# Optimization experiments

Hardware: AMD Instinct MI355X
Metric: run time of the kernel (lower is better)

## Reference

```python
import jax, jax.numpy as jnp
import numpy as np

H = 32        # num query heads
KVH = 8       # num kv heads
D = 128       # head_dim
ROPE_BASE = 10000.0
NEG_INF = jnp.finfo(jnp.float32).min


def rope_interleaved(x):
    """Interleaved (GPT-NeoX-style pairs (x0,x1),(x2,x3),...) RoPE. x: [b,s,h,d]."""
    d = x.shape[-1]
    inv_freq = 1.0 / (ROPE_BASE ** (jnp.arange(0, d, 2, dtype=jnp.float32) / d))  # [d/2]
    pos = jnp.arange(x.shape[1], dtype=jnp.float32)
    ang = pos[:, None] * inv_freq[None, :]                    # [s, d/2]
    cos = jnp.cos(ang)[None, :, None, :]
    sin = jnp.sin(ang)[None, :, None, :]
    xp = x.reshape(*x.shape[:-1], d // 2, 2)
    x1, x2 = xp[..., 0], xp[..., 1]
    r1 = x1 * cos - x2 * sin
    r2 = x1 * sin + x2 * cos
    return jnp.stack([r1, r2], axis=-1).reshape(x.shape)


def setup_inputs() -> dict:
    key = jax.random.key(0)
    k1, k2, k3 = jax.random.split(key, 3)
    B, S, E = 2, 2048, 4096
    x = jax.random.normal(k1, (B, S, E), dtype=jnp.float32)
    wqkv = jax.random.normal(k2, (E + 2 * KVH * D, E), dtype=jnp.float32) * 0.02
    wo = jax.random.normal(k3, (E, E), dtype=jnp.float32) * 0.02
    return {"x": x, "wqkv": wqkv, "wo": wo}


def reference(x, wqkv, wo):
    b, s, e = x.shape
    q_per_kv = H // KVH
    # fused QKV projection (torch Linear layout: y = x @ W.T)
    qkv = jnp.einsum('bse,fe->bsf', x, wqkv)
    # rearrange 'b s (h gs d) -> b s h gs d', gs = q_per_kv + 2
    qkv = qkv.reshape(b, s, KVH, q_per_kv + 2, D)
    q = qkv[..., :q_per_kv, :].reshape(b, s, H, D)   # (h gs) -> H query heads
    k = qkv[..., -2, :]                              # [b,s,KVH,D]
    v = qkv[..., -1, :]
    # RoPE (rotary_emb_dim == head_dim, interleaved)
    q = rope_interleaved(q)
    k = rope_interleaved(k)
    # GQA: expand kv heads to match query heads
    k = jnp.repeat(k, q_per_kv, axis=2)              # [b,s,H,D]
    v = jnp.repeat(v, q_per_kv, axis=2)
    scale = D ** -0.5
    scores = jnp.einsum('bqhd,bkhd->bhqk', q, k) * scale
    causal = jnp.tril(jnp.ones((s, s), dtype=bool))
    scores = jnp.where(causal[None, None], scores, NEG_INF)
    attn = jax.nn.softmax(scores, axis=-1)
    ctx = jnp.einsum('bhqk,bkhd->bqhd', attn, v).reshape(b, s, H * D)
    return jnp.einsum('bsf,ef->bse', ctx, wo)
```

## Files before the change

### kernel.cpp

```cpp
#include <hip/hip_runtime.h>
#include <cstdint>

typedef __bf16 bf16;
typedef __bf16 bf16x8 __attribute__((ext_vector_type(8)));
typedef float  f32x4  __attribute__((ext_vector_type(4)));

#define AS1(p) ((__attribute__((address_space(1))) void*)(p))
#define AS3(p) ((__attribute__((address_space(3))) void*)(p))

__device__ __forceinline__ void gload16(const void* g, void* l) {
  __builtin_amdgcn_global_load_lds(AS1(g), AS3(l), 16, 0, 0);
}

constexpr int B_ = 2, S_ = 2048, E_ = 4096, H_ = 32, KVH_ = 8, D_ = 128;
constexpr int QPK_ = H_ / KVH_;
constexpr int F_ = E_ + 2 * KVH_ * D_;
constexpr int M_ = B_ * S_;

__global__ void f2bf_k(const float* __restrict__ in, bf16* __restrict__ out, int n8) {
  int i = blockIdx.x * 256 + threadIdx.x;
  if (i >= n8) return;
  const float4* p = (const float4*)(in + (size_t)i * 8);
  float4 a = p[0], b = p[1];
  bf16x8 o;
  o[0] = (bf16)a.x; o[1] = (bf16)a.y; o[2] = (bf16)a.z; o[3] = (bf16)a.w;
  o[4] = (bf16)b.x; o[5] = (bf16)b.y; o[6] = (bf16)b.z; o[7] = (bf16)b.w;
  *(bf16x8*)(out + (size_t)i * 8) = o;
}

__global__ void rope_table_k(float2* __restrict__ tab) {
  int i = blockIdx.x * 256 + threadIdx.x;
  int s = i >> 6, f = i & 63;
  float inv = powf(10000.0f, -2.0f * (float)f / 128.0f);
  float ang = (float)s * inv;
  tab[i] = make_float2(cosf(ang), sinf(ang));
}

template <typename OutT>
__global__ __launch_bounds__(512, 2)
void gemm256(const bf16* __restrict__ A, const bf16* __restrict__ B,
             OutT* __restrict__ C, int M, int N, int K) {
  __shared__ bf16 As[2][16384];
  __shared__ bf16 Bs[2][16384];
  const int tid = threadIdx.x;
  const int wid = tid >> 6, lane = tid & 63;
  const int l15 = lane & 15, g = lane >> 4;
  const int wr = wid >> 2, wc = wid & 3;
  const int bm = blockIdx.x, bn = blockIdx.y;
  const bf16* Ab = A + (size_t)bm * 256 * K;
  const bf16* Bb = B + (size_t)bn * 256 * K;
  const int nT = K >> 6;
  const int swzr = (l15 & 7) << 4;

  f32x4 acc[8][4];
#pragma unroll
  for (int m = 0; m < 8; ++m)
#pragma unroll
    for (int n = 0; n < 4; ++n) acc[m][n] = (f32x4){0.f, 0.f, 0.f, 0.f};

  auto stg = [&](const bf16* src, bf16* dst, int t, int h) {
#pragma unroll
    for (int i = 0; i < 2; ++i) {
      int lb = h * 16384 + i * 8192 + wid * 1024 + lane * 16;
      int row = lb >> 7;
      int colb = (lb & 127) ^ ((row & 7) << 4);
      gload16(src + (size_t)row * K + t * 64 + (colb >> 1),
              dst + ((h * 16384 + i * 8192 + wid * 1024) >> 1));
    }
  };

  bf16x8 af[4][2];
  bf16x8 bfr[2][2][2];

  stg(Bb, Bs[0], 0, 0); stg(Bb, Bs[0], 0, 1);
  stg(Ab, As[0], 0, 0); stg(Ab, As[0], 0, 1);
  if (nT > 1) {
    stg(Bb, Bs[1], 1, 0); stg(Bb, Bs[1], 1, 1);
    asm volatile("s_waitcnt vmcnt(4)");
  } else {
    asm volatile("s_waitcnt vmcnt(0)");
  }
  __builtin_amdgcn_sched_barrier(0);
  __builtin_amdgcn_s_barrier();

  auto tileK = [&](int t, const int cur) {
#pragma unroll
    for (int m = 0; m < 4; ++m) {
      int arow = wr * 128 + m * 16 + l15;
#pragma unroll
      for (int ks = 0; ks < 2; ++ks)
        af[m][ks] = *(const bf16x8*)&As[cur][(arow << 6) + (((ks * 64 + g * 16) ^ swzr) >> 1)];
    }
#pragma unroll
    for (int n = 0; n < 2; ++n) {
      int brow = wc * 64 + n * 16 + l15;
#pragma unroll
      for (int ks = 0; ks < 2; ++ks)
        bfr[0][n][ks] = *(const bf16x8*)&Bs[cur][(brow << 6) + (((ks * 64 + g * 16) ^ swzr) >> 1)];
    }
    if (t + 1 < nT) stg(Ab, As[cur ^ 1], t + 1, 0);
    __builtin_amdgcn_s_barrier();
    asm volatile("s_waitcnt lgkmcnt(0)");
    __builtin_amdgcn_s_setprio(1);
#pragma unroll
    for (int ks = 0; ks < 2; ++ks)
#pragma unroll
      for (int m = 0; m < 4; ++m)
#pragma unroll
        for (int n = 0; n < 2; ++n)
          acc[m][n] = __builtin_amdgcn_mfma_f32_16x16x32_bf16(af[m][ks], bfr[0][n][ks], acc[m][n], 0, 0, 0);
    __builtin_amdgcn_s_setprio(0);
    __builtin_amdgcn_s_barrier();
#pragma unroll
    for (int n = 0; n < 2; ++n) {
      int brow = wc * 64 + 32 + n * 16 + l15;
#pragma unroll
      for (int ks = 0; ks < 2; ++ks)
        bfr[1][n][ks] = *(const bf16x8*)&Bs[cur][(brow << 6) + (((ks * 64 + g * 16) ^ swzr) >> 1)];
    }
    if (t + 1 < nT) stg(Ab, As[cur ^ 1], t + 1, 1);
    __builtin_amdgcn_s_barrier();
    asm volatile("s_waitcnt lgkmcnt(0)");
    __builtin_amdgcn_s_setprio(1);
#pragma unroll
    for (int ks = 0; ks < 2; ++ks)
#pragma unroll
      for (int m = 0; m < 4; ++m)
#pragma unroll
        for (int n = 0; n < 2; ++n)
          acc[m][2 + n] = __builtin_amdgcn_mfma_f32_16x16x32_bf16(af[m][ks], bfr[1][n][ks], acc[m][2 + n], 0, 0, 0);
    __builtin_amdgcn_s_setprio(0);
    __builtin_amdgcn_s_barrier();
#pragma unroll
    for (int m = 0; m < 4; ++m) {
      int arow = wr * 128 + 64 + m * 16 + l15;
#pragma unroll
      for (int ks = 0; ks < 2; ++ks)
        af[m][ks] = *(const bf16x8*)&As[cur][(arow << 6) + (((ks * 64 + g * 16) ^ swzr) >> 1)];
    }
    if (t + 2 < nT) stg(Bb, Bs[cur], t + 2, 0);
    __builtin_amdgcn_s_barrier();
    asm volatile("s_waitcnt lgkmcnt(0)");
    __builtin_amdgcn_s_setprio(1);
#pragma unroll
    for (int ks = 0; ks < 2; ++ks)
#pragma unroll
      for (int m = 0; m < 4; ++m)
#pragma unroll
        for (int n = 0; n < 2; ++n)
          acc[4 + m][n] = __builtin_amdgcn_mfma_f32_16x16x32_bf16(af[m][ks], bfr[0][n][ks], acc[4 + m][n], 0, 0, 0);
    __builtin_amdgcn_s_setprio(0);
    __builtin_amdgcn_s_barrier();
    if (t + 2 < nT) stg(Bb, Bs[cur], t + 2, 1);
    __builtin_amdgcn_s_setprio(1);
#pragma unroll
    for (int ks = 0; ks < 2; ++ks)
#pragma unroll
      for (int m = 0; m < 4; ++m)
#pragma unroll
        for (int n = 0; n < 2; ++n)
          acc[4 + m][2 + n] = __builtin_amdgcn_mfma_f32_16x16x32_bf16(af[m][ks], bfr[1][n][ks], acc[4 + m][2 + n], 0, 0, 0);
    __builtin_amdgcn_s_setprio(0);
    if (t + 2 < nT)      { asm volatile("s_waitcnt vmcnt(4)"); }
    else if (t + 1 < nT) { asm volatile("s_waitcnt vmcnt(0)"); }
    __builtin_amdgcn_sched_barrier(0);
    __builtin_amdgcn_s_barrier();
  };

  for (int tt = 0; tt < nT; tt += 2) {
    tileK(tt, 0);
    tileK(tt + 1, 1);
  }

#pragma unroll
  for (int mh = 0; mh < 2; ++mh)
#pragma unroll
    for (int m = 0; m < 4; ++m) {
      int row0 = bm * 256 + wr * 128 + mh * 64 + m * 16 + g * 4;
#pragma unroll
      for (int nh = 0; nh < 2; ++nh)
#pragma unroll
        for (int n = 0; n < 2; ++n) {
          int col = bn * 256 + wc * 64 + nh * 32 + n * 16 + l15;
          f32x4 v = acc[mh * 4 + m][nh * 2 + n];
#pragma unroll
          for (int r = 0; r < 4; ++r)
            C[(size_t)(row0 + r) * N + col] = (OutT)v[r];
        }
    }
}

__global__ void rope_q_k(const bf16* __restrict__ qkv, const float2* __restrict__ tab,
                         bf16* __restrict__ qout) {
  int idx = blockIdx.x * 256 + threadIdx.x;
  int c = idx & 15;
  int h = (idx >> 4) & 31;
  int s = (idx >> 9) & 2047;
  int b = idx >> 20;
  int d0 = c * 8;
  int kvh = h >> 2, j = h & 3;
  const bf16* src = qkv + (size_t)(b * 2048 + s) * F_ + kvh * (QPK_ + 2) * D_ + j * D_ + d0;
  bf16x8 v = *(const bf16x8*)src;
  const float2* tb = tab + s * 64 + (d0 >> 1);
  bf16x8 o;
#pragma unroll
  for (int p = 0; p < 4; ++p) {
    float x0 = (float)v[2 * p], x1 = (float)v[2 * p + 1];
    float2 cs = tb[p];
    o[2 * p]     = (bf16)(x0 * cs.x - x1 * cs.y);
    o[2 * p + 1] = (bf16)(x0 * cs.y + x1 * cs.x);
  }
  *(bf16x8*)(qout + (((size_t)b * 2048 + s) * 32 + h) * 128 + d0) = o;
}

__global__ void rope_k_k(const bf16* __restrict__ qkv, const float2* __restrict__ tab,
                         bf16* __restrict__ kout) {
  int idx = blockIdx.x * 256 + threadIdx.x;
  int c = idx & 15;
  int kvh = (idx >> 4) & 7;
  int s = (idx >> 7) & 2047;
  int b = idx >> 18;
  int d0 = c * 8;
  const bf16* src = qkv + (size_t)(b * 2048 + s) * F_ + kvh * (QPK_ + 2) * D_ + QPK_ * D_ + d0;
  bf16x8 v = *(const bf16x8*)src;
  const float2* tb = tab + s * 64 + (d0 >> 1);
  bf16x8 o;
#pragma unroll
  for (int p = 0; p < 4; ++p) {
    float x0 = (float)v[2 * p], x1 = (float)v[2 * p + 1];
    float2 cs = tb[p];
    o[2 * p]     = (bf16)(x0 * cs.x - x1 * cs.y);
    o[2 * p + 1] = (bf16)(x0 * cs.y + x1 * cs.x);
  }
  *(bf16x8*)(kout + ((size_t)(b * 8 + kvh) * 2048 + s) * 128 + d0) = o;
}

__global__ void vtrans_k(const bf16* __restrict__ qkv, bf16* __restrict__ vt) {
  int bidx = blockIdx.x;
  int st = bidx & 31;
  int dt = (bidx >> 5) & 3;
  int kvh = (bidx >> 7) & 7;
  int b = bidx >> 10;
  __shared__ bf16 tile[64][40];
  int t = threadIdx.x;
  {
    int sl = t >> 2, d0 = (t & 3) * 8;
    bf16x8 v = *(const bf16x8*)(qkv + (size_t)(b * 2048 + st * 64 + sl) * F_ +
                                kvh * (QPK_ + 2) * D_ + (QPK_ + 1) * D_ + dt * 32 + d0);
#pragma unroll
    for (int i = 0; i < 8; ++i) tile[sl][d0 + i] = v[i];
  }
  __syncthreads();
  {
    int dl = t >> 3, s0 = (t & 7) * 8;
    bf16x8 o;
#pragma unroll
    for (int i = 0; i < 8; ++i) o[i] = tile[s0 + i][dl];
    *(bf16x8*)(vt + ((size_t)(b * 8 + kvh) * 128 + dt * 32 + dl) * 2048 + st * 64 + s0) = o;
  }
}

__global__ __launch_bounds__(512, 2)
void attn_k(const bf16* __restrict__ q, const bf16* __restrict__ k,
            const bf16* __restrict__ vt, bf16* __restrict__ ctx) {
  int bid = blockIdx.x;
  bid = (bid & 7) * 64 + (bid >> 3);
  int qp = bid & 7;
  int h = (bid >> 3) & 31;
  int b = bid >> 8;
  int kvh = h >> 2;
  int tid = threadIdx.x, w = tid >> 6, lane = tid & 63;
  int l15 = lane & 15, g = lane >> 4;

  __shared__ bf16 Ks[3][64 * 128];
  __shared__ bf16 Vs[3][128 * 64];
  __shared__ bf16 Plds[8][16 * 80];

  bf16* Pw = &Plds[w][0];
  const float C2 = 0.08838834764831845f * 1.4426950408889634f;
  const float NEG = -3.0e38f;

  const bf16* kb_base = k + (size_t)(b * 8 + kvh) * 2048 * 128;
  const bf16* vt_base = vt + (size_t)(b * 8 + kvh) * 128 * 2048;

  auto stage = [&](int kv0, int buf) {
#pragma unroll
    for (int i = 0; i < 2; ++i) {
      int lt = i * 8192 + tid * 16;
      int row = lt >> 8;
      int ch = (lt >> 4) & 15;
      int srcel = (ch ^ (row & 7)) << 3;
      gload16(kb_base + (size_t)(kv0 + row) * 128 + srcel,
              &Ks[buf][(i * 8192 + w * 1024) >> 1]);
    }
#pragma unroll
    for (int i = 0; i < 2; ++i) {
      int lt = i * 8192 + tid * 16;
      int row = lt >> 7;
      int ch = (lt >> 4) & 7;
      int srcel = (ch ^ (row & 7)) << 3;
      gload16(vt_base + (size_t)row * 2048 + kv0 + srcel,
              &Vs[buf][(i * 8192 + w * 1024) >> 1]);
    }
  };

  const int kxor = (l15 & 7) << 4;

  for (int pass = 0; pass < 2; ++pass) {
    int qt = pass ? (15 - qp) : qp;
    int qrow0 = qt * 128 + w * 16;

    bf16x8 aq[4];
#pragma unroll
    for (int ks = 0; ks < 4; ++ks)
      aq[ks] = *(const bf16x8*)(q + (((size_t)b * 2048 + qrow0 + l15) * 32 + h) * 128 + ks * 32 + g * 8);

    f32x4 acco[8];
#pragma unroll
    for (int n = 0; n < 8; ++n) acco[n] = (f32x4){0.f, 0.f, 0.f, 0.f};
    float m_r[4] = {NEG, NEG, NEG, NEG};
    float l_r[4] = {0.f, 0.f, 0.f, 0.f};

    const int nk = 2 * qt + 2;
    stage(0, 0);
    stage(64, 1);
    asm volatile("s_waitcnt vmcnt(4)");
    __builtin_amdgcn_sched_barrier(0);
    __builtin_amdgcn_s_barrier();

    for (int kt = 0; kt < nk; ++kt) {
      int kv0 = kt * 64;
      int cur = kt % 3;
      if (kt + 2 < nk) stage(kv0 + 128, (kt + 2) % 3);

      if (kv0 <= qrow0 + 15) {
        f32x4 s[4];
#pragma unroll
        for (int n = 0; n < 4; ++n) s[n] = (f32x4){0.f, 0.f, 0.f, 0.f};
#pragma unroll
        for (int ks = 0; ks < 4; ++ks) {
          int off = ((ks * 64 + g * 16) ^ kxor) >> 1;
#pragma unroll
          for (int n = 0; n < 4; ++n) {
            bf16x8 kb = *(const bf16x8*)&Ks[cur][(n * 16 + l15) * 128 + off];
            s[n] = __builtin_amdgcn_mfma_f32_16x16x32_bf16(aq[ks], kb, s[n], 0, 0, 0);
          }
        }
        if (kv0 + 63 > qrow0) {
#pragma unroll
          for (int n = 0; n < 4; ++n)
#pragma unroll
            for (int r = 0; r < 4; ++r) {
              int qg = qrow0 + g * 4 + r;
              int kg = kv0 + n * 16 + l15;
              if (kg > qg) s[n][r] = NEG;
            }
        }
        float fac[4];
#pragma unroll
        for (int r = 0; r < 4; ++r) {
          float mx = fmaxf(fmaxf(s[0][r], s[1][r]), fmaxf(s[2][r], s[3][r]));
#pragma unroll
          for (int off = 1; off < 16; off <<= 1) mx = fmaxf(mx, __shfl_xor(mx, off));
          float mn = fmaxf(m_r[r], mx);
          fac[r] = exp2f((m_r[r] - mn) * C2);
          m_r[r] = mn;
        }
        float psum[4] = {0.f, 0.f, 0.f, 0.f};
#pragma unroll
        for (int n = 0; n < 4; ++n)
#pragma unroll
          for (int r = 0; r < 4; ++r) {
            float p = exp2f((s[n][r] - m_r[r]) * C2);
            psum[r] += p;
            Pw[(g * 4 + r) * 80 + n * 16 + l15] = (bf16)p;
          }
#pragma unroll
        for (int r = 0; r < 4; ++r) {
          float ps = psum[r];
#pragma unroll
          for (int off = 1; off < 16; off <<= 1) ps += __shfl_xor(ps, off);
          l_r[r] = l_r[r] * fac[r] + ps;
        }
#pragma unroll
        for (int n = 0; n < 8; ++n)
#pragma unroll
          for (int r = 0; r < 4; ++r) acco[n][r] *= fac[r];
        __builtin_amdgcn_sched_barrier(0);
        asm volatile("s_waitcnt lgkmcnt(0)");
        __builtin_amdgcn_sched_barrier(0);
#pragma unroll
        for (int ks = 0; ks < 2; ++ks) {
          bf16x8 pa = *(const bf16x8*)&Pw[l15 * 80 + ks * 32 + g * 8];
          int off = ((ks * 64 + g * 16) ^ kxor) >> 1;
#pragma unroll
          for (int n = 0; n < 8; ++n) {
            bf16x8 vb = *(const bf16x8*)&Vs[cur][(n * 16 + l15) * 64 + off];
            acco[n] = __builtin_amdgcn_mfma_f32_16x16x32_bf16(pa, vb, acco[n], 0, 0, 0);
          }
        }
      }

      if (kt + 1 < nk) {
        if (kt + 2 < nk) { asm volatile("s_waitcnt vmcnt(4)"); }
        else             { asm volatile("s_waitcnt vmcnt(0)"); }
        __builtin_amdgcn_sched_barrier(0);
      }
      __builtin_amdgcn_s_barrier();
    }

#pragma unroll
    for (int r = 0; r < 4; ++r) {
      float inv = 1.0f / l_r[r];
      int qg = qrow0 + g * 4 + r;
#pragma unroll
      for (int n = 0; n < 8; ++n)
        ctx[(((size_t)b * 2048 + qg) * 32 + h) * 128 + n * 16 + l15] = (bf16)(acco[n][r] * inv);
    }
  }
}

extern "C" void kernel_launch(void* const* d_in, const int* in_sizes, int n_in,
                              void* d_out, int out_size, void* d_ws, size_t ws_size,
                              hipStream_t stream) {
  const float* x = (const float*)d_in[0];
  const float* wqkv = (const float*)d_in[1];
  const float* wo = (const float*)d_in[2];
  float* out = (float*)d_out;
  char* ws = (char*)d_ws;

  bf16* xbf    = (bf16*)(ws + 0);
  bf16* wqkvbf = (bf16*)(ws + 33554432);
  bf16* qkvbf  = (bf16*)(ws + 83886080);
  bf16* qbuf   = (bf16*)(ws + 134217728);
  bf16* kbuf   = (bf16*)(ws + 167772160);
  bf16* vtbuf  = (bf16*)(ws + 176160768);
  float2* tab  = (float2*)(ws + 184549376);

  f2bf_k<<<8192, 256, 0, stream>>>(x, xbf, M_ * E_ / 8);
  f2bf_k<<<12288, 256, 0, stream>>>(wqkv, wqkvbf, F_ * E_ / 8);
  rope_table_k<<<512, 256, 0, stream>>>(tab);

  gemm256<bf16><<<dim3(M_ / 256, F_ / 256), 512, 0, stream>>>(xbf, wqkvbf, qkvbf, M_, F_, E_);

  rope_q_k<<<8192, 256, 0, stream>>>(qkvbf, tab, qbuf);
  rope_k_k<<<2048, 256, 0, stream>>>(qkvbf, tab, kbuf);
  vtrans_k<<<2048, 256, 0, stream>>>(qkvbf, vtbuf);

  bf16* wobf = qkvbf;
  f2bf_k<<<8192, 256, 0, stream>>>(wo, wobf, E_ * E_ / 8);

  bf16* ctx = xbf;
  attn_k<<<512, 512, 0, stream>>>(qbuf, kbuf, vtbuf, ctx);

  gemm256<float><<<dim3(M_ / 256, E_ / 256), 512, 0, stream>>>(ctx, wobf, out, M_, E_, E_);
}
```

Measured before the change: 590.0 us.

## Triple-buffer B tiles and load all A fragments per K-step in GEMM

```diff
diff --git a/kernel.cpp b/kernel.cpp
--- a/kernel.cpp
+++ b/kernel.cpp
@@ -41,7 +41,7 @@
 void gemm256(const bf16* __restrict__ A, const bf16* __restrict__ B,
              OutT* __restrict__ C, int M, int N, int K) {
   __shared__ bf16 As[2][16384];
-  __shared__ bf16 Bs[2][16384];
+  __shared__ bf16 Bs[3][16384];
   const int tid = threadIdx.x;
   const int wid = tid >> 6, lane = tid & 63;
   const int l15 = lane & 15, g = lane >> 4;
@@ -58,57 +58,64 @@
 #pragma unroll
     for (int n = 0; n < 4; ++n) acc[m][n] = (f32x4){0.f, 0.f, 0.f, 0.f};
 
-  auto stg = [&](const bf16* src, bf16* dst, int t, int h) {
-#pragma unroll
-    for (int i = 0; i < 2; ++i) {
-      int lb = h * 16384 + i * 8192 + wid * 1024 + lane * 16;
+  auto stgA = [&](int t) {
+#pragma unroll
+    for (int i = 0; i < 4; ++i) {
+      int lb = i * 8192 + wid * 1024 + lane * 16;
       int row = lb >> 7;
       int colb = (lb & 127) ^ ((row & 7) << 4);
-      gload16(src + (size_t)row * K + t * 64 + (colb >> 1),
-              dst + ((h * 16384 + i * 8192 + wid * 1024) >> 1));
+      gload16(Ab + (size_t)row * K + t * 64 + (colb >> 1),
+              &As[t & 1][(i * 8192 + wid * 1024) >> 1]);
     }
   };
-
-  bf16x8 af[4][2];
-  bf16x8 bfr[2][2][2];
-
-  stg(Bb, Bs[0], 0, 0); stg(Bb, Bs[0], 0, 1);
-  stg(Ab, As[0], 0, 0); stg(Ab, As[0], 0, 1);
-  if (nT > 1) {
-    stg(Bb, Bs[1], 1, 0); stg(Bb, Bs[1], 1, 1);
-    asm volatile("s_waitcnt vmcnt(4)");
-  } else {
-    asm volatile("s_waitcnt vmcnt(0)");
-  }
+  auto stgB = [&](int t) {
+    bf16* dst = &Bs[t % 3][0];
+#pragma unroll
+    for (int i = 0; i < 4; ++i) {
+      int lb = i * 8192 + wid * 1024 + lane * 16;
+      int row = lb >> 7;
+      int colb = (lb & 127) ^ ((row & 7) << 4);
+      gload16(Bb + (size_t)row * K + t * 64 + (colb >> 1),
+              dst + ((i * 8192 + wid * 1024) >> 1));
+    }
+  };
+
+  stgB(0); stgA(0);
+  if (nT > 1) { stgB(1); asm volatile("s_waitcnt vmcnt(4)"); }
+  else        { asm volatile("s_waitcnt vmcnt(0)"); }
   __builtin_amdgcn_sched_barrier(0);
   __builtin_amdgcn_s_barrier();
 
-  auto tileK = [&](int t, const int cur) {
-#pragma unroll
-    for (int m = 0; m < 4; ++m) {
+  bf16x8 af[8][2], blo[2][2], bhi[2][2];
+  for (int t = 0; t < nT; ++t) {
+    const bf16* Asc = &As[t & 1][0];
+    const bf16* Bsc = &Bs[t % 3][0];
+#pragma unroll
+    for (int m = 0; m < 8; ++m) {
       int arow = wr * 128 + m * 16 + l15;
 #pragma unroll
       for (int ks = 0; ks < 2; ++ks)
-        af[m][ks] = *(const bf16x8*)&As[cur][(arow << 6) + (((ks * 64 + g * 16) ^ swzr) >> 1)];
+        af[m][ks] = *(const bf16x8*)&Asc[(arow << 6) + (((ks * 64 + g * 16) ^ swzr) >> 1)];
     }
 #pragma unroll
     for (int n = 0; n < 2; ++n) {
       int brow = wc * 64 + n * 16 + l15;
 #pragma unroll
       for (int ks = 0; ks < 2; ++ks)
-        bfr[0][n][ks] = *(const bf16x8*)&Bs[cur][(brow << 6) + (((ks * 64 + g * 16) ^ swzr) >> 1)];
-    }
-    if (t + 1 < nT) stg(Ab, As[cur ^ 1], t + 1, 0);
+        blo[n][ks] = *(const bf16x8*)&Bsc[(brow << 6) + (((ks * 64 + g * 16) ^ swzr) >> 1)];
+    }
+    if (t + 1 < nT) stgA(t + 1);
     __builtin_amdgcn_s_barrier();
     asm volatile("s_waitcnt lgkmcnt(0)");
+    __builtin_amdgcn_sched_barrier(0);
     __builtin_amdgcn_s_setprio(1);
 #pragma unroll
     for (int ks = 0; ks < 2; ++ks)
 #pragma unroll
-      for (int m = 0; m < 4; ++m)
+      for (int m = 0; m < 8; ++m)
 #pragma unroll
         for (int n = 0; n < 2; ++n)
-          acc[m][n] = __builtin_amdgcn_mfma_f32_16x16x32_bf16(af[m][ks], bfr[0][n][ks], acc[m][n], 0, 0, 0);
+          acc[m][n] = __builtin_amdgcn_mfma_f32_16x16x32_bf16(af[m][ks], blo[n][ks], acc[m][n], 0, 0, 0);
     __builtin_amdgcn_s_setprio(0);
     __builtin_amdgcn_s_barrier();
 #pragma unroll
@@ -116,78 +123,39 @@
       int brow = wc * 64 + 32 + n * 16 + l15;
 #pragma unroll
       for (int ks = 0; ks < 2; ++ks)
-        bfr[1][n][ks] = *(const bf16x8*)&Bs[cur][(brow << 6) + (((ks * 64 + g * 16) ^ swzr) >> 1)];
-    }
-    if (t + 1 < nT) stg(Ab, As[cur ^ 1], t + 1, 1);
+        bhi[n][ks] = *(const bf16x8*)&Bsc[(brow << 6) + (((ks * 64 + g * 16) ^ swzr) >> 1)];
+    }
+    if (t + 2 < nT) stgB(t + 2);
     __builtin_amdgcn_s_barrier();
     asm volatile("s_waitcnt lgkmcnt(0)");
+    __builtin_amdgcn_sched_barrier(0);
     __builtin_amdgcn_s_setprio(1);
 #pragma unroll
     for (int ks = 0; ks < 2; ++ks)
 #pragma unroll
-      for (int m = 0; m < 4; ++m)
+      for (int m = 0; m < 8; ++m)
 #pragma unroll
         for (int n = 0; n < 2; ++n)
-          acc[m][2 + n] = __builtin_amdgcn_mfma_f32_16x16x32_bf16(af[m][ks], bfr[1][n][ks], acc[m][2 + n], 0, 0, 0);
-    __builtin_amdgcn_s_setprio(0);
-    __builtin_amdgcn_s_barrier();
-#pragma unroll
-    for (int m = 0; m < 4; ++m) {
-      int arow = wr * 128 + 64 + m * 16 + l15;
-#pragma unroll
-      for (int ks = 0; ks < 2; ++ks)
-        af[m][ks] = *(const bf16x8*)&As[cur][(arow << 6) + (((ks * 64 + g * 16) ^ swzr) >> 1)];
-    }
-    if (t + 2 < nT) stg(Bb, Bs[cur], t + 2, 0);
-    __builtin_amdgcn_s_barrier();
-    asm volatile("s_waitcnt lgkmcnt(0)");
-    __builtin_amdgcn_s_setprio(1);
-#pragma unroll
-    for (int ks = 0; ks < 2; ++ks)
-#pragma unroll
-      for (int m = 0; m < 4; ++m)
-#pragma unroll
-        for (int n = 0; n < 2; ++n)
-          acc[4 + m][n] = __builtin_amdgcn_mfma_f32_16x16x32_bf16(af[m][ks], bfr[0][n][ks], acc[4 + m][n], 0, 0, 0);
-    __builtin_amdgcn_s_setprio(0);
-    __builtin_amdgcn_s_barrier();
-    if (t + 2 < nT) stg(Bb, Bs[cur], t + 2, 1);
-    __builtin_amdgcn_s_setprio(1);
-#pragma unroll
-    for (int ks = 0; ks < 2; ++ks)
-#pragma unroll
-      for (int m = 0; m < 4; ++m)
-#pragma unroll
-        for (int n = 0; n < 2; ++n)
-          acc[4 + m][2 + n] = __builtin_amdgcn_mfma_f32_16x16x32_bf16(af[m][ks], bfr[1][n][ks], acc[4 + m][2 + n], 0, 0, 0);
+          acc[m][2 + n] = __builtin_amdgcn_mfma_f32_16x16x32_bf16(af[m][ks], bhi[n][ks], acc[m][2 + n], 0, 0, 0);
     __builtin_amdgcn_s_setprio(0);
     if (t + 2 < nT)      { asm volatile("s_waitcnt vmcnt(4)"); }
     else if (t + 1 < nT) { asm volatile("s_waitcnt vmcnt(0)"); }
     __builtin_amdgcn_sched_barrier(0);
     __builtin_amdgcn_s_barrier();
-  };
-
-  for (int tt = 0; tt < nT; tt += 2) {
-    tileK(tt, 0);
-    tileK(tt + 1, 1);
-  }
-
-#pragma unroll
-  for (int mh = 0; mh < 2; ++mh)
-#pragma unroll
-    for (int m = 0; m < 4; ++m) {
-      int row0 = bm * 256 + wr * 128 + mh * 64 + m * 16 + g * 4;
-#pragma unroll
-      for (int nh = 0; nh < 2; ++nh)
-#pragma unroll
-        for (int n = 0; n < 2; ++n) {
-          int col = bn * 256 + wc * 64 + nh * 32 + n * 16 + l15;
-          f32x4 v = acc[mh * 4 + m][nh * 2 + n];
-#pragma unroll
-          for (int r = 0; r < 4; ++r)
-            C[(size_t)(row0 + r) * N + col] = (OutT)v[r];
-        }
-    }
+  }
+
+#pragma unroll
+  for (int m = 0; m < 8; ++m) {
+    int row0 = bm * 256 + wr * 128 + m * 16 + g * 4;
+#pragma unroll
+    for (int ni = 0; ni < 4; ++ni) {
+      int col = bn * 256 + wc * 64 + ni * 16 + l15;
+      f32x4 v = acc[m][ni];
+#pragma unroll
+      for (int r = 0; r < 4; ++r)
+        C[(size_t)(row0 + r) * N + col] = (OutT)v[r];
+    }
+  }
 }
 
 __global__ void rope_q_k(const bf16* __restrict__ qkv, const float2* __restrict__ tab,
```

Result: no change. 593.0 us (+0.5%).
